# Optimization experiments

Hardware: AMD Instinct MI355X
Metric: run time of the kernel (lower is better)

## Reference

```python
import jax, jax.numpy as jnp
import numpy as np

B, NUM_GENES, F = 8, 20000, 128
N, E, H = 50000, 800000, 128


def setup_inputs() -> dict:
    key = jax.random.key(0)
    k = jax.random.split(key, 8)
    gene_emb = jax.random.normal(k[0], (B, NUM_GENES, F), dtype=jnp.float32)
    W1 = jax.random.normal(k[1], (F, H), dtype=jnp.float32) * 0.05
    b1 = jnp.zeros((H,), dtype=jnp.float32)
    W2 = jax.random.normal(k[2], (H, H), dtype=jnp.float32) * 0.05
    b2 = jnp.zeros((H,), dtype=jnp.float32)
    global_ids = jax.random.randint(k[3], (N,), 0, NUM_GENES, dtype=jnp.int64)
    edge_index = jax.random.randint(k[4], (2, E), 0, N, dtype=jnp.int64)
    return {"gene_emb": gene_emb, "W1": W1, "b1": b1, "W2": W2, "b2": b2,
            "global_ids": global_ids, "edge_index": edge_index}


def reference(gene_emb, W1, b1, W2, b2, global_ids, edge_index):
    n = global_ids.shape[0]
    # GCN normalization with self-loops (PyG GCNConv default):
    # A_hat = A + I, deg over target nodes, norm = d^{-1/2}[src] * d^{-1/2}[dst]
    loop = jnp.arange(n)
    src = jnp.concatenate([edge_index[0], loop])  # [E+N]
    dst = jnp.concatenate([edge_index[1], loop])  # [E+N]
    deg = jnp.zeros((n,), gene_emb.dtype).at[dst].add(1.0)
    dinv = jax.lax.rsqrt(deg)  # deg >= 1 thanks to self-loops
    norm = (dinv[src] * dinv[dst])[None, :, None]  # [1, E+N, 1]

    def gcn(x, W, b):
        h = x @ W                                   # [B, N, H] transform first (linear commutes)
        msg = h[:, src, :] * norm                   # gather + scale: [B, E+N, H]
        agg = jnp.zeros_like(h).at[:, dst].add(msg)  # scatter-add over targets
        return agg + b

    x = gene_emb[:, global_ids, :]                  # [B, N, F] node feature gather
    x = jax.nn.relu(gcn(x, W1, b1))
    x = gcn(x, W2, b2)
    # global_mean_pool: each batch replica is one whole graph -> mean over nodes
    return x.mean(axis=1)                           # [B, H]
```

## Files before the change

### kernel.cpp

```cpp
#include <hip/hip_runtime.h>

#define NG 20000
#define BB 8
#define FD 128
#define HA 1000
#define HB 300

typedef unsigned int uint;
typedef unsigned short ushort;
typedef __attribute__((ext_vector_type(8))) short short8v;
typedef __attribute__((ext_vector_type(4))) float float4v;
typedef __attribute__((ext_vector_type(4))) int int4v;
typedef __attribute__((ext_vector_type(2))) float f2v;

__device__ f2v llvm_rbl_v2f32(int4v srsrc, int voffset, int soffset, int aux)
    __asm("llvm.amdgcn.raw.buffer.load.v2f32");

__device__ __forceinline__ int4v make_srsrc(const void* p) {
    int4v r;
    r.x = (int)(uint)(uintptr_t)p;
    r.y = (int)(uint)((uintptr_t)p >> 32);
    r.z = -1;
    r.w = 0x00020000;
    return r;
}

__device__ __forceinline__ ushort f2bf(float x) {
    uint u = __float_as_uint(x);
    u += 0x7FFFu + ((u >> 16) & 1u);
    return (ushort)(u >> 16);
}
__device__ __forceinline__ float bf_lo(uint u) { return __uint_as_float(u << 16); }
__device__ __forceinline__ float bf_hi(uint u) { return __uint_as_float(u & 0xFFFF0000u); }

__device__ __forceinline__ void h_tile(char* smem, int hb,
                                       const float* __restrict__ gene,
                                       const ushort* __restrict__ w1t,
                                       uint* __restrict__ h2u, int t) {
    ushort* Al = (ushort*)smem;
    ushort* Bl = (ushort*)(smem + 16384);
    float*  Cl = (float*)smem;
    int p  = hb & 3;
    int g0 = (hb >> 2) * 32;

#pragma unroll
    for (int s = 0; s < 8; s++) {
        int f = t + s * 256;
        int r = f >> 5, k0 = (f & 31) * 4;
        int bb = 2 * p + (r >> 5);
        int gg = g0 + (r & 31);
        float4 v = *(const float4*)(gene + ((size_t)bb * NG + gg) * 128 + k0);
        ushort4 u;
        u.x = f2bf(v.x); u.y = f2bf(v.y); u.z = f2bf(v.z); u.w = f2bf(v.w);
        int byte = (r * 256 + k0 * 2) ^ ((r & 7) << 4);
        *(ushort4*)(smem + byte) = u;
    }
#pragma unroll
    for (int s = 0; s < 8; s++) {
        int f = t + s * 256;
        int j = f >> 4, k0 = (f & 15) * 8;
        uint4 v = *(const uint4*)(w1t + j * 128 + k0);
        int byte = (j * 256 + k0 * 2) ^ ((j & 7) << 4);
        *(uint4*)((char*)Bl + byte) = v;
    }
    __syncthreads();

    int wid = t >> 6, lane = t & 63;
    int r0 = wid * 16;
    int lrow = lane & 15, lhi = lane >> 4;
    float4v acc[8];
#pragma unroll
    for (int nf = 0; nf < 8; nf++) acc[nf] = (float4v)(0.f);

#pragma unroll
    for (int c = 0; c < 4; c++) {
        int ra = r0 + lrow;
        int byteA = (ra * 256 + (c * 32 + lhi * 8) * 2) ^ ((ra & 7) << 4);
        short8v a = *(short8v*)((char*)Al + byteA);
#pragma unroll
        for (int nf = 0; nf < 8; nf++) {
            int jb = nf * 16 + lrow;
            int byteB = (jb * 256 + (c * 32 + lhi * 8) * 2) ^ ((jb & 7) << 4);
            short8v b = *(short8v*)((char*)Bl + byteB);
            acc[nf] = __builtin_amdgcn_mfma_f32_16x16x32_bf16(a, b, acc[nf], 0, 0, 0);
        }
    }
    __syncthreads();

#pragma unroll
    for (int nf = 0; nf < 8; nf++) {
#pragma unroll
        for (int q = 0; q < 4; q++) {
            Cl[(r0 + lhi * 4 + q) * 128 + nf * 16 + lrow] = acc[nf][q];
        }
    }
    __syncthreads();

#pragma unroll
    for (int s = 0; s < 16; s++) {
        int flat = t + s * 256;
        int gi = flat >> 7, cc = flat & 127;
        float lo = Cl[gi * 128 + cc];
        float hi = Cl[(32 + gi) * 128 + cc];
        uint u = (uint)f2bf(lo) | ((uint)f2bf(hi) << 16);
        h2u[((size_t)p * NG + g0 + gi) * 128 + cc] = u;
    }
}

__global__ void k_setup(int* ideg, float* s_acc, int* ticket,
                        const float* __restrict__ W1, ushort* w1t, int N) {
    int i = blockIdx.x * blockDim.x + threadIdx.x;
    if (i < N) ideg[i] = 0;
    if (i < 8 * BB * FD) s_acc[i] = 0.0f;
    if (i == 0) *ticket = 0;
    if (i < FD * FD) {
        int j = i >> 7, k = i & 127;
        w1t[i] = f2bf(W1[k * 128 + j]);
    }
}

__global__ __launch_bounds__(256, 3)
void k_counth(const int* __restrict__ dst, int* ideg, int* epos, int E, int eb,
              const float* __restrict__ gene, const ushort* __restrict__ w1t,
              uint* __restrict__ h2u) {
    __shared__ __align__(16) char smem[49152];
    if ((int)blockIdx.x < eb) {
        int e = blockIdx.x * 256 + threadIdx.x;
        if (e < E) epos[e] = atomicAdd(&ideg[dst[e]], 1);
        return;
    }
    h_tile(smem, blockIdx.x - eb, gene, w1t, h2u, threadIdx.x);
}

__global__ __launch_bounds__(256, 3)
void k_scanh(const int* __restrict__ ideg, float* dinv, float* cval,
             int* padcnt, int* offs, const int* __restrict__ gid,
             int2* csr, int* ticket, int N, int nb,
             const float* __restrict__ gene, const ushort* __restrict__ w1t,
             uint* __restrict__ h2u) {
    __shared__ __align__(16) char smem[49152];
    if ((int)blockIdx.x >= nb) {
        h_tile(smem, (int)blockIdx.x - nb + HA, gene, w1t, h2u, threadIdx.x);
        return;
    }
    int* sd = (int*)smem;
    __shared__ int sbase;
    int t = threadIdx.x, idx = blockIdx.x * 256 + t;
    int v = 0, d = 0;
    float iv = 0.f;
    if (idx < N) {
        d = ideg[idx] + 1;
        float fd = (float)d;
        dinv[idx] = rsqrtf(fd);
        iv = 1.0f / fd;
        cval[idx] = iv;
        v = (d + 7) & ~7;
        padcnt[idx] = v;
    }
    sd[t] = v; __syncthreads();
    for (int o = 1; o < 256; o <<= 1) {
        int x = (t >= o) ? sd[t - o] : 0;
        __syncthreads();
        sd[t] += x;
        __syncthreads();
    }
    if (t == 255) sbase = atomicAdd(ticket, sd[255]);
    __syncthreads();
    if (idx < N) {
        int o = sbase + sd[t] - v;
        offs[idx] = o;
        csr[o] = make_int2(gid[idx], __float_as_int(iv));
        for (int z = d; z < v; z++) csr[o + z] = make_int2(0, 0);
    }
}

__global__ __launch_bounds__(256, 3)
void k_fillh(const int* __restrict__ src, const int* __restrict__ dst,
             const int* __restrict__ gid, const float* __restrict__ dinv,
             float* cval, const int* __restrict__ offs,
             const int* __restrict__ epos,
             int2* csr, int E, int eb,
             const float* __restrict__ gene, const ushort* __restrict__ w1t,
             uint* __restrict__ h2u) {
    __shared__ __align__(16) char smem[49152];
    if ((int)blockIdx.x < eb) {
        int e = blockIdx.x * 256 + threadIdx.x;
        if (e >= E) return;
        int s = src[e], d = dst[e];
        float nrm = dinv[s] * dinv[d];
        atomicAdd(&cval[s], nrm);
        csr[offs[d] + 1 + epos[e]] = make_int2(gid[s], __float_as_int(nrm));
        return;
    }
    h_tile(smem, (int)blockIdx.x - eb + HA + HB, gene, w1t, h2u, threadIdx.x);
}

__global__ __launch_bounds__(512)
void k_aggp(const uint* __restrict__ hp, const int2* __restrict__ csr,
            const int* __restrict__ offs, const int* __restrict__ padcnt,
            const float* __restrict__ cval, const float* __restrict__ b1,
            float* __restrict__ s_acc, int N, int wpp) {
    int p    = blockIdx.x & 3;
    int wid  = threadIdx.x >> 6, lane = threadIdx.x & 63;
    int w    = __builtin_amdgcn_readfirstlane((blockIdx.x >> 2) * 8 + wid);
    int4v sr = make_srsrc(hp + (size_t)p * NG * 128);
    int voff = lane * 8;
    int l2 = lane * 2;
    float bx = b1[l2], by = b1[l2 + 1];
    float sx0 = 0.f, sx1 = 0.f, sy0 = 0.f, sy1 = 0.f;

    int i0 = (int)((long long)w * N / wpp);
    int i1 = (int)((long long)(w + 1) * N / wpp);
    for (int i = i0; i < i1; ++i) {
        int   e  = offs[i];
        int   pc = padcnt[i];
        float cv = cval[i];
        float ax0 = 0.f, ax1 = 0.f, ay0 = 0.f, ay1 = 0.f;
        for (int q = 0; q < pc; q += 8) {
            int ee = e + q;
            int2 c0 = csr[ee],     c1 = csr[ee + 1], c2 = csr[ee + 2], c3 = csr[ee + 3];
            int2 c4 = csr[ee + 4], c5 = csr[ee + 5], c6 = csr[ee + 6], c7 = csr[ee + 7];
            f2v u0 = llvm_rbl_v2f32(sr, voff, c0.x << 9, 0);
            f2v u1 = llvm_rbl_v2f32(sr, voff, c1.x << 9, 0);
            f2v u2 = llvm_rbl_v2f32(sr, voff, c2.x << 9, 0);
            f2v u3 = llvm_rbl_v2f32(sr, voff, c3.x << 9, 0);
            f2v u4 = llvm_rbl_v2f32(sr, voff, c4.x << 9, 0);
            f2v u5 = llvm_rbl_v2f32(sr, voff, c5.x << 9, 0);
            f2v u6 = llvm_rbl_v2f32(sr, voff, c6.x << 9, 0);
            f2v u7 = llvm_rbl_v2f32(sr, voff, c7.x << 9, 0);
            float n0 = __int_as_float(c0.y), n1 = __int_as_float(c1.y);
            float n2 = __int_as_float(c2.y), n3 = __int_as_float(c3.y);
            float n4 = __int_as_float(c4.y), n5 = __int_as_float(c5.y);
            float n6 = __int_as_float(c6.y), n7 = __int_as_float(c7.y);
            uint a, b;
            a = __float_as_uint(u0.x); b = __float_as_uint(u0.y);
            ax0 = fmaf(n0, bf_lo(a), ax0); ax1 = fmaf(n0, bf_hi(a), ax1);
            ay0 = fmaf(n0, bf_lo(b), ay0); ay1 = fmaf(n0, bf_hi(b), ay1);
            a = __float_as_uint(u1.x); b = __float_as_uint(u1.y);
            ax0 = fmaf(n1, bf_lo(a), ax0); ax1 = fmaf(n1, bf_hi(a), ax1);
            ay0 = fmaf(n1, bf_lo(b), ay0); ay1 = fmaf(n1, bf_hi(b), ay1);
            a = __float_as_uint(u2.x); b = __float_as_uint(u2.y);
            ax0 = fmaf(n2, bf_lo(a), ax0); ax1 = fmaf(n2, bf_hi(a), ax1);
            ay0 = fmaf(n2, bf_lo(b), ay0); ay1 = fmaf(n2, bf_hi(b), ay1);
            a = __float_as_uint(u3.x); b = __float_as_uint(u3.y);
            ax0 = fmaf(n3, bf_lo(a), ax0); ax1 = fmaf(n3, bf_hi(a), ax1);
            ay0 = fmaf(n3, bf_lo(b), ay0); ay1 = fmaf(n3, bf_hi(b), ay1);
            a = __float_as_uint(u4.x); b = __float_as_uint(u4.y);
            ax0 = fmaf(n4, bf_lo(a), ax0); ax1 = fmaf(n4, bf_hi(a), ax1);
            ay0 = fmaf(n4, bf_lo(b), ay0); ay1 = fmaf(n4, bf_hi(b), ay1);
            a = __float_as_uint(u5.x); b = __float_as_uint(u5.y);
            ax0 = fmaf(n5, bf_lo(a), ax0); ax1 = fmaf(n5, bf_hi(a), ax1);
            ay0 = fmaf(n5, bf_lo(b), ay0); ay1 = fmaf(n5, bf_hi(b), ay1);
            a = __float_as_uint(u6.x); b = __float_as_uint(u6.y);
            ax0 = fmaf(n6, bf_lo(a), ax0); ax1 = fmaf(n6, bf_hi(a), ax1);
            ay0 = fmaf(n6, bf_lo(b), ay0); ay1 = fmaf(n6, bf_hi(b), ay1);
            a = __float_as_uint(u7.x); b = __float_as_uint(u7.y);
            ax0 = fmaf(n7, bf_lo(a), ax0); ax1 = fmaf(n7, bf_hi(a), ax1);
            ay0 = fmaf(n7, bf_lo(b), ay0); ay1 = fmaf(n7, bf_hi(b), ay1);
        }
        sx0 += cv * fmaxf(ax0 + bx, 0.f);
        sx1 += cv * fmaxf(ax1 + bx, 0.f);
        sy0 += cv * fmaxf(ay0 + by, 0.f);
        sy1 += cv * fmaxf(ay1 + by, 0.f);
    }

    __shared__ float red[8][256];
    red[wid][lane * 4 + 0] = sx0;
    red[wid][lane * 4 + 1] = sx1;
    red[wid][lane * 4 + 2] = sy0;
    red[wid][lane * 4 + 3] = sy1;
    __syncthreads();
    int t = threadIdx.x;
    if (t < 256) {
        float s = 0.f;
#pragma unroll
        for (int wv = 0; wv < 8; wv++) s += red[wv][t];
        int l = t >> 2, c = t & 3;
        int rep = (blockIdx.x >> 2) & 7;
        atomicAdd(&s_acc[rep * 1024 + (2 * p + (c & 1)) * 128 + 2 * l + (c >> 1)], s);
    }
}

__global__ void k_final(const float* __restrict__ s_acc, const float* __restrict__ W2,
                        const float* __restrict__ b2, float* __restrict__ out, float invN) {
    __shared__ float ss[1024];
    int t = threadIdx.x;
    for (int idx = t; idx < 1024; idx += 128) {
        float s = 0.f;
#pragma unroll
        for (int r = 0; r < 8; r++) s += s_acc[r * 1024 + idx];
        ss[idx] = s;
    }
    __syncthreads();
    float acc[8];
#pragma unroll
    for (int b = 0; b < 8; b++) acc[b] = 0.f;
    for (int k = 0; k < 128; k++) {
        float w = W2[k * 128 + t];
#pragma unroll
        for (int b = 0; b < 8; b++) acc[b] += ss[b * 128 + k] * w;
    }
    float bb = b2[t];
#pragma unroll
    for (int b = 0; b < 8; b++) out[b * 128 + t] = acc[b] * invN + bb;
}


extern "C" void kernel_launch(void* const* d_in, const int* in_sizes, int n_in,
                              void* d_out, int out_size, void* d_ws, size_t ws_size,
                              hipStream_t stream) {
    const float* gene = (const float*)d_in[0];
    const float* W1   = (const float*)d_in[1];
    const float* b1   = (const float*)d_in[2];
    const float* W2   = (const float*)d_in[3];
    const float* b2   = (const float*)d_in[4];
    const int*   gid  = (const int*)d_in[5];
    const int*   eidx = (const int*)d_in[6];
    int N = in_sizes[5];
    int E = in_sizes[6] / 2;
    const int* src = eidx;
    const int* dst = eidx + E;
    float* out = (float*)d_out;

    char* p = (char*)d_ws;
    auto alloc = [&](size_t bytes) -> char* {
        char* r = p; p += (bytes + 255) & ~(size_t)255; return r;
    };
    size_t csr_cap = (size_t)E + 8 * (size_t)N;
    int*   ideg   = (int*)  alloc((size_t)N * 4);
    float* dinv   = (float*)alloc((size_t)N * 4);
    float* cval   = (float*)alloc((size_t)N * 4);
    int*   padcnt = (int*)  alloc((size_t)N * 4);
    int*   offs   = (int*)  alloc((size_t)N * 4);
    int*   epos   = (int*)  alloc((size_t)E * 4);
    int*   ticket = (int*)  alloc(256);
    int2*  csr    = (int2*) alloc(csr_cap * 8);
    float* s_acc  = (float*)alloc(8 * 1024 * 4);
    uint*  h2     = (uint*) alloc((size_t)NG * BB * FD * 2);
    ushort* w1t   = (ushort*)alloc(128 * 128 * 2);

    int nb = (N + 255) / 256;
    int eb = (E + 255) / 256;
    int hblk = 4 * (NG / 32);

    const int NBLK = 2048;
    int wpp = (NBLK / 4) * 8;

    k_setup <<<nb, 256, 0, stream>>>(ideg, s_acc, ticket, W1, w1t, N);
    k_counth<<<eb + HA, 256, 0, stream>>>(dst, ideg, epos, E, eb, gene, w1t, h2);
    k_scanh <<<nb + HB, 256, 0, stream>>>(ideg, dinv, cval, padcnt, offs, gid,
                                          csr, ticket, N, nb, gene, w1t, h2);
    k_fillh <<<eb + (hblk - HA - HB), 256, 0, stream>>>(src, dst, gid, dinv, cval, offs,
                                                        epos, csr, E, eb, gene, w1t, h2);
    k_aggp  <<<NBLK, 512, 0, stream>>>(h2, csr, offs, padcnt,
                                       cval, b1, s_acc, N, wpp);
    k_final <<<1, 128, 0, stream>>>(s_acc, W2, b2, out, 1.0f / (float)N);
}
```

Measured before the change: 275.2 us.

## Reschedule H-tile GEMM across kernels, splitting aggregation per batch pair

Work is now split by batch pair. Pairs 0 and 1 of the projected features are computed in the count and fill kernels. Pairs 2 and 3 are computed inside the first two aggregation launches by a new 512-thread tile routine, while those launches aggregate the pairs that are already finished. The scan kernel no longer carries GEMM work. This is meant to balance the GEMM tiles against the edge and aggregation phases and hide them behind the memory-bound gather. In exchange it adds two more kernel launches and makes the aggregation per pair less parallel, since 1024 blocks cover each pair separately.

```diff
diff --git a/kernel.cpp b/kernel.cpp
--- a/kernel.cpp
+++ b/kernel.cpp
@@ -3,8 +3,8 @@
 #define NG 20000
 #define BB 8
 #define FD 128
-#define HA 1000
-#define HB 300
+#define GT 625
+#define NAB 1024
 
 typedef unsigned int uint;
 typedef unsigned short ushort;
@@ -71,7 +71,6 @@
     float4v acc[8];
 #pragma unroll
     for (int nf = 0; nf < 8; nf++) acc[nf] = (float4v)(0.f);
-
 #pragma unroll
     for (int c = 0; c < 4; c++) {
         int ra = r0 + lrow;
@@ -86,7 +85,6 @@
         }
     }
     __syncthreads();
-
 #pragma unroll
     for (int nf = 0; nf < 8; nf++) {
 #pragma unroll
@@ -95,10 +93,81 @@
         }
     }
     __syncthreads();
-
 #pragma unroll
     for (int s = 0; s < 16; s++) {
         int flat = t + s * 256;
+        int gi = flat >> 7, cc = flat & 127;
+        float lo = Cl[gi * 128 + cc];
+        float hi = Cl[(32 + gi) * 128 + cc];
+        uint u = (uint)f2bf(lo) | ((uint)f2bf(hi) << 16);
+        h2u[((size_t)p * NG + g0 + gi) * 128 + cc] = u;
+    }
+}
+
+__device__ __forceinline__ void h_tile512(char* smem, int hb,
+                                          const float* __restrict__ gene,
+                                          const ushort* __restrict__ w1t,
+                                          uint* __restrict__ h2u, int t) {
+    ushort* Al = (ushort*)smem;
+    ushort* Bl = (ushort*)(smem + 16384);
+    float*  Cl = (float*)smem;
+    int p  = hb & 3;
+    int g0 = (hb >> 2) * 32;
+
+#pragma unroll
+    for (int s = 0; s < 4; s++) {
+        int f = t + s * 512;
+        int r = f >> 5, k0 = (f & 31) * 4;
+        int bb = 2 * p + (r >> 5);
+        int gg = g0 + (r & 31);
+        float4 v = *(const float4*)(gene + ((size_t)bb * NG + gg) * 128 + k0);
+        ushort4 u;
+        u.x = f2bf(v.x); u.y = f2bf(v.y); u.z = f2bf(v.z); u.w = f2bf(v.w);
+        int byte = (r * 256 + k0 * 2) ^ ((r & 7) << 4);
+        *(ushort4*)(smem + byte) = u;
+    }
+#pragma unroll
+    for (int s = 0; s < 4; s++) {
+        int f = t + s * 512;
+        int j = f >> 4, k0 = (f & 15) * 8;
+        uint4 v = *(const uint4*)(w1t + j * 128 + k0);
+        int byte = (j * 256 + k0 * 2) ^ ((j & 7) << 4);
+        *(uint4*)((char*)Bl + byte) = v;
+    }
+    __syncthreads();
+
+    int wid = t >> 6, lane = t & 63;
+    int r0 = (wid & 3) * 16;
+    int nf0 = (wid >> 2) * 4;
+    int lrow = lane & 15, lhi = lane >> 4;
+    float4v acc[4];
+#pragma unroll
+    for (int j = 0; j < 4; j++) acc[j] = (float4v)(0.f);
+#pragma unroll
+    for (int c = 0; c < 4; c++) {
+        int ra = r0 + lrow;
+        int byteA = (ra * 256 + (c * 32 + lhi * 8) * 2) ^ ((ra & 7) << 4);
+        short8v a = *(short8v*)((char*)Al + byteA);
+#pragma unroll
+        for (int j = 0; j < 4; j++) {
+            int jb = (nf0 + j) * 16 + lrow;
+            int byteB = (jb * 256 + (c * 32 + lhi * 8) * 2) ^ ((jb & 7) << 4);
+            short8v b = *(short8v*)((char*)Bl + byteB);
+            acc[j] = __builtin_amdgcn_mfma_f32_16x16x32_bf16(a, b, acc[j], 0, 0, 0);
+        }
+    }
+    __syncthreads();
+#pragma unroll
+    for (int j = 0; j < 4; j++) {
+#pragma unroll
+        for (int q = 0; q < 4; q++) {
+            Cl[(r0 + lhi * 4 + q) * 128 + (nf0 + j) * 16 + lrow] = acc[j][q];
+        }
+    }
+    __syncthreads();
+#pragma unroll
+    for (int s = 0; s < 8; s++) {
+        int flat = t + s * 512;
         int gi = flat >> 7, cc = flat & 127;
         float lo = Cl[gi * 128 + cc];
         float hi = Cl[(32 + gi) * 128 + cc];
@@ -129,21 +198,13 @@
         if (e < E) epos[e] = atomicAdd(&ideg[dst[e]], 1);
         return;
     }
-    h_tile(smem, blockIdx.x - eb, gene, w1t, h2u, threadIdx.x);
-}
-
-__global__ __launch_bounds__(256, 3)
-void k_scanh(const int* __restrict__ ideg, float* dinv, float* cval,
-             int* padcnt, int* offs, const int* __restrict__ gid,
-             int2* csr, int* ticket, int N, int nb,
-             const float* __restrict__ gene, const ushort* __restrict__ w1t,
-             uint* __restrict__ h2u) {
-    __shared__ __align__(16) char smem[49152];
-    if ((int)blockIdx.x >= nb) {
-        h_tile(smem, (int)blockIdx.x - nb + HA, gene, w1t, h2u, threadIdx.x);
-        return;
-    }
-    int* sd = (int*)smem;
+    h_tile(smem, ((int)blockIdx.x - eb) * 4 + 0, gene, w1t, h2u, threadIdx.x);
+}
+
+__global__ void k_scan(const int* __restrict__ ideg, float* dinv, float* cval,
+                       int* padcnt, int* offs, const int* __restrict__ gid,
+                       int2* csr, int* ticket, int N) {
+    __shared__ int sd[256];
     __shared__ int sbase;
     int t = threadIdx.x, idx = blockIdx.x * 256 + t;
     int v = 0, d = 0;
@@ -192,17 +253,17 @@
         csr[offs[d] + 1 + epos[e]] = make_int2(gid[s], __float_as_int(nrm));
         return;
     }
-    h_tile(smem, (int)blockIdx.x - eb + HA + HB, gene, w1t, h2u, threadIdx.x);
-}
-
-__global__ __launch_bounds__(512)
-void k_aggp(const uint* __restrict__ hp, const int2* __restrict__ csr,
-            const int* __restrict__ offs, const int* __restrict__ padcnt,
-            const float* __restrict__ cval, const float* __restrict__ b1,
-            float* __restrict__ s_acc, int N, int wpp) {
-    int p    = blockIdx.x & 3;
+    h_tile(smem, ((int)blockIdx.x - eb) * 4 + 1, gene, w1t, h2u, threadIdx.x);
+}
+
+__device__ __forceinline__ void aggp_body(
+        int p, int bid, const uint* __restrict__ hp, const int2* __restrict__ csr,
+        const int* __restrict__ offs, const int* __restrict__ padcnt,
+        const float* __restrict__ cval, const float* __restrict__ b1,
+        float* __restrict__ s_acc, int N, float* red) {
     int wid  = threadIdx.x >> 6, lane = threadIdx.x & 63;
-    int w    = __builtin_amdgcn_readfirstlane((blockIdx.x >> 2) * 8 + wid);
+    int w    = __builtin_amdgcn_readfirstlane(bid * 8 + wid);
+    const int wpp = NAB * 8;
     int4v sr = make_srsrc(hp + (size_t)p * NG * 128);
     int voff = lane * 8;
     int l2 = lane * 2;
@@ -264,21 +325,44 @@
         sy1 += cv * fmaxf(ay1 + by, 0.f);
     }
 
-    __shared__ float red[8][256];
-    red[wid][lane * 4 + 0] = sx0;
-    red[wid][lane * 4 + 1] = sx1;
-    red[wid][lane * 4 + 2] = sy0;
-    red[wid][lane * 4 + 3] = sy1;
+    red[wid * 256 + lane * 4 + 0] = sx0;
+    red[wid * 256 + lane * 4 + 1] = sx1;
+    red[wid * 256 + lane * 4 + 2] = sy0;
+    red[wid * 256 + lane * 4 + 3] = sy1;
     __syncthreads();
     int t = threadIdx.x;
     if (t < 256) {
         float s = 0.f;
 #pragma unroll
-        for (int wv = 0; wv < 8; wv++) s += red[wv][t];
+        for (int wv = 0; wv < 8; wv++) s += red[wv * 256 + t];
         int l = t >> 2, c = t & 3;
-        int rep = (blockIdx.x >> 2) & 7;
+        int rep = bid & 7;
         atomicAdd(&s_acc[rep * 1024 + (2 * p + (c & 1)) * 128 + 2 * l + (c >> 1)], s);
     }
+}
+
+__global__ __launch_bounds__(512)
+void k_aggph(int p, int hpair, const uint* __restrict__ hp, const int2* __restrict__ csr,
+             const int* __restrict__ offs, const int* __restrict__ padcnt,
+             const float* __restrict__ cval, const float* __restrict__ b1,
+             float* __restrict__ s_acc, int N,
+             const float* __restrict__ gene, const ushort* __restrict__ w1t,
+             uint* __restrict__ h2u) {
+    __shared__ __align__(16) char smem[49152];
+    if ((int)blockIdx.x >= NAB) {
+        h_tile512(smem, ((int)blockIdx.x - NAB) * 4 + hpair, gene, w1t, h2u, threadIdx.x);
+        return;
+    }
+    aggp_body(p, blockIdx.x, hp, csr, offs, padcnt, cval, b1, s_acc, N, (float*)smem);
+}
+
+__global__ __launch_bounds__(512)
+void k_aggp2(int p, const uint* __restrict__ hp, const int2* __restrict__ csr,
+             const int* __restrict__ offs, const int* __restrict__ padcnt,
+             const float* __restrict__ cval, const float* __restrict__ b1,
+             float* __restrict__ s_acc, int N) {
+    __shared__ float red[8 * 256];
+    aggp_body(p, blockIdx.x, hp, csr, offs, padcnt, cval, b1, s_acc, N, red);
 }
 
 __global__ void k_final(const float* __restrict__ s_acc, const float* __restrict__ W2,
@@ -341,18 +425,18 @@
 
     int nb = (N + 255) / 256;
     int eb = (E + 255) / 256;
-    int hblk = 4 * (NG / 32);
-
-    const int NBLK = 2048;
-    int wpp = (NBLK / 4) * 8;
 
     k_setup <<<nb, 256, 0, stream>>>(ideg, s_acc, ticket, W1, w1t, N);
-    k_counth<<<eb + HA, 256, 0, stream>>>(dst, ideg, epos, E, eb, gene, w1t, h2);
-    k_scanh <<<nb + HB, 256, 0, stream>>>(ideg, dinv, cval, padcnt, offs, gid,
-                                          csr, ticket, N, nb, gene, w1t, h2);
-    k_fillh <<<eb + (hblk - HA - HB), 256, 0, stream>>>(src, dst, gid, dinv, cval, offs,
-                                                        epos, csr, E, eb, gene, w1t, h2);
-    k_aggp  <<<NBLK, 512, 0, stream>>>(h2, csr, offs, padcnt,
-                                       cval, b1, s_acc, N, wpp);
+    k_counth<<<eb + GT, 256, 0, stream>>>(dst, ideg, epos, E, eb, gene, w1t, h2);
+    k_scan  <<<nb, 256, 0, stream>>>(ideg, dinv, cval, padcnt, offs, gid,
+                                     csr, ticket, N);
+    k_fillh <<<eb + GT, 256, 0, stream>>>(src, dst, gid, dinv, cval, offs,
+                                          epos, csr, E, eb, gene, w1t, h2);
+    k_aggph <<<NAB + GT, 512, 0, stream>>>(0, 2, h2, csr, offs, padcnt,
+                                           cval, b1, s_acc, N, gene, w1t, h2);
+    k_aggph <<<NAB + GT, 512, 0, stream>>>(1, 3, h2, csr, offs, padcnt,
+                                           cval, b1, s_acc, N, gene, w1t, h2);
+    k_aggp2 <<<NAB, 512, 0, stream>>>(2, h2, csr, offs, padcnt, cval, b1, s_acc, N);
+    k_aggp2 <<<NAB, 512, 0, stream>>>(3, h2, csr, offs, padcnt, cval, b1, s_acc, N);
     k_final <<<1, 128, 0, stream>>>(s_acc, W2, b2, out, 1.0f / (float)N);
 }
```

Measured after the change: 307.1 us. 1.12x slower.
